# Kernel tuning notes

Measured on AMD Instinct MI355X. Metric: run time of the kernel, lower is better.

The kernel has to match this reference:

```python
import jax, jax.numpy as jnp
import numpy as np

D_MODEL = 1024
NUM_HEAD = 16
BATCH = 2
SEQ = 2048
NEG_INF = -1e9  # matches masked_fill value in the original


def setup_inputs() -> dict:
    key = jax.random.key(0)
    k1, k2, k3, k4, k5 = jax.random.split(key, 5)
    scale = 1.0 / np.sqrt(D_MODEL)
    return {
        "x": jax.random.normal(k1, (BATCH, SEQ, D_MODEL), dtype=jnp.float32),
        "q_weight": jax.random.normal(k2, (D_MODEL, D_MODEL), dtype=jnp.float32) * scale,
        "k_weight": jax.random.normal(k3, (D_MODEL, D_MODEL), dtype=jnp.float32) * scale,
        "v_weight": jax.random.normal(k4, (D_MODEL, D_MODEL), dtype=jnp.float32) * scale,
        "o_weight": jax.random.normal(k5, (D_MODEL, D_MODEL), dtype=jnp.float32) * scale,
    }


def reference(x, q_weight, k_weight, v_weight, o_weight):
    b, s, d = x.shape
    h = NUM_HEAD
    dh = d // h
    # projections: weight layout is (d_out, d_in)
    q = jnp.einsum('bsd,ed->bse', x, q_weight).reshape(b, s, h, dh).transpose(0, 2, 1, 3)
    k = jnp.einsum('bsd,ed->bse', x, k_weight).reshape(b, s, h, dh).transpose(0, 2, 1, 3)
    v = jnp.einsum('bsd,ed->bse', x, v_weight).reshape(b, s, h, dh).transpose(0, 2, 1, 3)
    scores = jnp.einsum('bhqd,bhkd->bhqk', q, k) / jnp.sqrt(jnp.asarray(dh, x.dtype))
    causal = jnp.triu(jnp.ones((s, s), dtype=bool), k=1)  # True above diagonal -> masked
    scores = jnp.where(causal, jnp.asarray(NEG_INF, x.dtype), scores)
    attn = jax.nn.softmax(scores, axis=-1)
    out = jnp.einsum('bhqk,bhkd->bhqd', attn, v)          # [b,h,s,dh]
    out = out.transpose(0, 2, 1, 3).reshape(b, s, d)       # merge heads
    return jnp.einsum('bse,de->bsd', out, o_weight)
```

## Files before the change

kernel.cpp:

```cpp
#include <hip/hip_runtime.h>

typedef short bhalf8 __attribute__((ext_vector_type(8)));
typedef short short4v __attribute__((ext_vector_type(4)));
typedef unsigned uint4v __attribute__((ext_vector_type(4)));
typedef float floatx4 __attribute__((ext_vector_type(4)));

#define D_MODEL 1024
#define SEQ     2048
#define BATCH   2
#define NHEAD   16
#define DH      64

#define GLDS(g, l) __builtin_amdgcn_global_load_lds( \
    (const __attribute__((address_space(1))) void*)(g), \
    (__attribute__((address_space(3))) void*)(l), 16, 0, 0)

static __device__ __forceinline__ short f2bf(float f) {
    unsigned u = __builtin_bit_cast(unsigned, f);
    u = (u + 0x7fffu + ((u >> 16) & 1u)) >> 16;
    return (short)u;
}
static __device__ __forceinline__ unsigned pack2(float a, float b) {
    return (unsigned)(unsigned short)f2bf(a) | ((unsigned)(unsigned short)f2bf(b) << 16);
}
static __device__ __forceinline__ unsigned cvt_pk_bf16(float lo, float hi) {
    unsigned r;
    asm("v_cvt_pk_bf16_f32 %0, %1, %2" : "=v"(r) : "v"(lo), "v"(hi));
    return r;
}

__global__ __launch_bounds__(256) void cast_all(const float* __restrict__ x,
                                                const float* __restrict__ wq,
                                                const float* __restrict__ wk,
                                                const float* __restrict__ wv,
                                                const float* __restrict__ wo,
                                                short* __restrict__ xb,
                                                short* __restrict__ wall) {
    const int bid = blockIdx.x;
    const float* s;
    short* d;
    int i;
    if (bid < 2048) {
        s = x; d = xb;
        i = (bid * 256 + threadIdx.x) * 8;
    } else {
        const int wb = bid - 2048;
        const int which = wb >> 9;
        s = (which == 0) ? wq : (which == 1) ? wk : (which == 2) ? wv : wo;
        d = wall + (size_t)which * (D_MODEL * D_MODEL);
        i = ((wb & 511) * 256 + threadIdx.x) * 8;
    }
    float4 a = *(const float4*)(s + i);
    float4 b = *(const float4*)(s + i + 4);
    uint4 u = {pack2(a.x, a.y), pack2(a.z, a.w), pack2(b.x, b.y), pack2(b.z, b.w)};
    *(uint4*)(d + i) = u;
}

#define MFMA_BF16 __builtin_amdgcn_mfma_f32_16x16x32_bf16

#define QISSUE(kt, s) do {                                                    \
    char* ab_ = pool + (s) * 16384 + (w * 32) * 64;                           \
    char* bb_ = pool + 49152 + (s) * 16384 + (w * 32) * 64;                   \
    GLDS(Ag + (size_t)(kt) * 32, ab_);                                        \
    GLDS(Ag + (size_t)(kt) * 32 + 16 * 1024, ab_ + 1024);                     \
    GLDS(Wg + (size_t)(kt) * 32, bb_);                                        \
    GLDS(Wg + (size_t)(kt) * 32 + 16 * 1024, bb_ + 1024);                     \
} while (0)

#define QCOMP(s) do {                                                         \
    const short(*As_)[32] = (const short(*)[32])(pool + (s) * 16384);         \
    const short(*Bs_)[32] = (const short(*)[32])(pool + 49152 + (s) * 16384); \
    bhalf8 af_[8], bf_[4];                                                    \
    _Pragma("unroll")                                                         \
    for (int m_ = 0; m_ < 8; ++m_)                                            \
        af_[m_] = *(const bhalf8*)&As_[wr * 128 + m_ * 16 + l16][quad * 8];   \
    _Pragma("unroll")                                                         \
    for (int n_ = 0; n_ < 4; ++n_)                                            \
        bf_[n_] = *(const bhalf8*)&Bs_[wc * 64 + n_ * 16 + l16][quad * 8];    \
    __builtin_amdgcn_s_setprio(1);                                            \
    _Pragma("unroll")                                                         \
    for (int m_ = 0; m_ < 8; ++m_)                                            \
        _Pragma("unroll")                                                     \
        for (int n_ = 0; n_ < 4; ++n_)                                        \
            acc[m_][n_] = MFMA_BF16(af_[m_], bf_[n_], acc[m_][n_], 0, 0, 0);  \
    __builtin_amdgcn_s_setprio(0);                                            \
} while (0)

__global__ __launch_bounds__(512) void gemm_qkv2(const short* __restrict__ A,
                                                 const short* __restrict__ W,
                                                 short* __restrict__ Qo,
                                                 short* __restrict__ Ko,
                                                 short* __restrict__ Vt) {
    __shared__ __align__(16) char pool[98304];
    const int t    = threadIdx.x;
    const int w    = t >> 6, lane = t & 63, quad = lane >> 4, l16 = lane & 15;
    const int wr   = w >> 2, wc = w & 3;
    const int bm   = blockIdx.x * 256;
    const int by   = (int)blockIdx.y;
    const int bn   = by * 256;

    const short* Ag = A + (size_t)(bm + w * 32 + (lane >> 2)) * 1024 + (lane & 3) * 8;
    const short* Wg = W + (size_t)(bn + w * 32 + (lane >> 2)) * 1024 + (lane & 3) * 8;

    floatx4 acc[8][4];
#pragma unroll
    for (int m = 0; m < 8; ++m)
#pragma unroll
        for (int n = 0; n < 4; ++n) {
            floatx4 z = {0.f, 0.f, 0.f, 0.f};
            acc[m][n] = z;
        }

    QISSUE(0, 0);
    QISSUE(1, 1);
    int sc_ = 0, sn_ = 2;
#pragma unroll 1
    for (int kt = 0; kt < 30; ++kt) {
        asm volatile("s_waitcnt vmcnt(4)" ::: "memory");
        __builtin_amdgcn_s_barrier();
        QISSUE(kt + 2, sn_);
        QCOMP(sc_);
        sc_ = (sc_ == 2) ? 0 : sc_ + 1;
        sn_ = (sn_ == 2) ? 0 : sn_ + 1;
    }
    asm volatile("s_waitcnt vmcnt(4)" ::: "memory");
    __builtin_amdgcn_s_barrier();
    QCOMP(sc_);
    sc_ = (sc_ == 2) ? 0 : sc_ + 1;
    asm volatile("s_waitcnt vmcnt(0)" ::: "memory");
    __builtin_amdgcn_s_barrier();
    QCOMP(sc_);

    __syncthreads();
    short (*Ct)[268] = (short(*)[268])pool;
    if (by < 8) {
        short* outp = (by < 4) ? Qo : Ko;
        const int colbase = (by < 4) ? bn : bn - 1024;
        for (int hh = 0; hh < 2; ++hh) {
            if (wr == hh) {
#pragma unroll
                for (int m = 0; m < 8; ++m)
#pragma unroll
                    for (int n = 0; n < 4; ++n)
#pragma unroll
                        for (int g = 0; g < 4; ++g)
                            Ct[m * 16 + quad * 4 + g][wc * 64 + n * 16 + l16] =
                                f2bf(acc[m][n][g]);
            }
            __syncthreads();
            {
                const int r = t >> 2, c0 = (t & 3) * 64;
#pragma unroll
                for (int p = 0; p < 8; ++p)
                    *(uint4*)(outp + (size_t)(bm + hh * 128 + r) * 1024 +
                              colbase + c0 + p * 8) =
                        *(const uint4*)&Ct[r][c0 + p * 8];
            }
            __syncthreads();
        }
    } else {
        const int nbase = bn - 2048;
        for (int hh = 0; hh < 2; ++hh) {
            if ((wc >> 1) == hh) {
#pragma unroll
                for (int m = 0; m < 8; ++m)
#pragma unroll
                    for (int n = 0; n < 4; ++n)
#pragma unroll
                        for (int g = 0; g < 4; ++g)
                            Ct[wc * 64 + n * 16 + l16 - hh * 128]
                              [wr * 128 + m * 16 + quad * 4 + g] =
                                f2bf(acc[m][n][g]);
            }
            __syncthreads();
            {
                const int r = t >> 2, c0 = (t & 3) * 64;
#pragma unroll
                for (int p = 0; p < 8; ++p)
                    *(uint4*)(Vt + (size_t)(nbase + hh * 128 + r) * 4096 +
                              bm + c0 + p * 8) =
                        *(const uint4*)&Ct[r][c0 + p * 8];
            }
            __syncthreads();
        }
    }
}

__global__ __launch_bounds__(256) void gemm_o(const short* __restrict__ A,
                                              const short* __restrict__ W,
                                              float* __restrict__ C) {
    __shared__ __align__(16) char pool[34816];
    short (*As)[64] = (short(*)[64])pool;
    short (*Bs)[64] = (short(*)[64])(pool + 16384);
    const int t    = threadIdx.x;
    const int wave = t >> 6, lane = t & 63, quad = lane >> 4, l16 = lane & 15;
    const int bm = blockIdx.x * 128, bn = blockIdx.y * 64;
    const int qm = (wave >> 1) * 64, qn = (wave & 1) * 32;

    const int lrow = lane >> 3, lcol = (lane & 7) * 8;
    const short* Ag = A + (size_t)(bm + wave * 32 + lrow) * 1024 + lcol;
    const short* Wg = W + (size_t)(bn + wave * 16 + lrow) * 1024 + lcol;
    short* Al = &As[wave * 32][0];
    short* Bl = &Bs[wave * 16][0];

    floatx4 acc[4][2];
#pragma unroll
    for (int i = 0; i < 4; ++i)
#pragma unroll
        for (int j = 0; j < 2; ++j) {
            floatx4 z = {0.f, 0.f, 0.f, 0.f};
            acc[i][j] = z;
        }

    for (int k0 = 0; k0 < 1024; k0 += 64) {
        __syncthreads();
#pragma unroll
        for (int j = 0; j < 4; ++j)
            GLDS(Ag + k0 + (size_t)j * 8 * 1024, Al + j * 8 * 64);
#pragma unroll
        for (int j = 0; j < 2; ++j)
            GLDS(Wg + k0 + (size_t)j * 8 * 1024, Bl + j * 8 * 64);
        __syncthreads();
#pragma unroll
        for (int kk = 0; kk < 64; kk += 32) {
            bhalf8 af[4], bfr[2];
#pragma unroll
            for (int im = 0; im < 4; ++im)
                af[im] = *(const bhalf8*)&As[qm + im * 16 + l16][kk + quad * 8];
#pragma unroll
            for (int jn = 0; jn < 2; ++jn)
                bfr[jn] = *(const bhalf8*)&Bs[qn + jn * 16 + l16][kk + quad * 8];
#pragma unroll
            for (int im = 0; im < 4; ++im)
#pragma unroll
                for (int jn = 0; jn < 2; ++jn)
                    acc[im][jn] = __builtin_amdgcn_mfma_f32_16x16x32_bf16(
                        af[im], bfr[jn], acc[im][jn], 0, 0, 0);
        }
    }

    __syncthreads();
    float (*Ctf)[68] = (float(*)[68])pool;
#pragma unroll
    for (int im = 0; im < 4; ++im)
#pragma unroll
        for (int jn = 0; jn < 2; ++jn)
#pragma unroll
            for (int g = 0; g < 4; ++g)
                Ctf[qm + im * 16 + quad * 4 + g][qn + jn * 16 + l16] = acc[im][jn][g];
    __syncthreads();
#pragma unroll
    for (int pass = 0; pass < 8; ++pass) {
        const int r = (t >> 4) + pass * 16;
        const int c = (t & 15) * 4;
        float4 u = *(const float4*)&Ctf[r][c];
        *(float4*)(C + (size_t)(bm + r) * 1024 + bn + c) = u;
    }
}


__global__ __launch_bounds__(512) void attn_v17(const short* __restrict__ Qo,
                                                const short* __restrict__ Ko,
                                                const short* __restrict__ Vt,
                                                short* __restrict__ Y) {
    __shared__ __align__(16) short Ks[2][64][72];
    __shared__ __align__(16) short Vs[2][64][72];

    const int t    = threadIdx.x;
    const int wave = t >> 6, lane = t & 63, quad = lane >> 4, l16 = lane & 15;
    const int bid  = (int)blockIdx.x;
    const int bh   = bid & 31;
    const int p    = (bid & 255) >> 5;
    const int qt   = (bid < 256) ? (15 - p) : p;
    const int b = bh >> 4, h = bh & 15;
    const int nc   = (qt + 1) * 2;

    const short* Qbase = Qo + (size_t)b * SEQ * 1024 + h * 64;
    const short* Kbase = Ko + (size_t)b * SEQ * 1024 + h * 64;
    const short* Vbase = Vt + (size_t)h * 64 * 4096 + (size_t)b * SEQ;

    const int sr = t >> 3;
    const int sc = (t & 7) * 8;

    const float KS = 0.125f * 1.44269504f;
    const float CB = 12.0f * 1.44269504f;

    const int qw_  = qt * 128 + wave * 16;
    const int qrow = qw_ + l16;
    const short* qr = Qbase + (size_t)qrow * 1024;
    bhalf8 qf0 = *(const bhalf8*)(qr + quad * 8);
    bhalf8 qf1 = *(const bhalf8*)(qr + 32 + quad * 8);

    float lsum = 0.f;
    floatx4 o[4];
#pragma unroll
    for (int nd = 0; nd < 4; ++nd) {
        floatx4 z = {0.f, 0.f, 0.f, 0.f};
        o[nd] = z;
    }

    uint4 kreg, vreg;
    kreg = *(const uint4*)(Kbase + (size_t)sr * 1024 + sc);
    vreg = *(const uint4*)(Vbase + (size_t)sr * 4096 + sc);
    *(uint4*)&Ks[0][sr][sc] = kreg;
    *(uint4*)&Vs[0][sr][sc] = vreg;
    if (nc > 1) {
        kreg = *(const uint4*)(Kbase + (size_t)(64 + sr) * 1024 + sc);
        vreg = *(const uint4*)(Vbase + (size_t)sr * 4096 + 64 + sc);
    }
    __syncthreads();

#pragma unroll 1
    for (int i = 0; i < nc; ++i) {
        const int buf = i & 1;
        if (i + 1 < nc) {
            *(uint4*)&Ks[buf ^ 1][sr][sc] = kreg;
            *(uint4*)&Vs[buf ^ 1][sr][sc] = vreg;
        }
        if (i + 2 < nc) {
            const int kn = (i + 2) * 64;
            kreg = *(const uint4*)(Kbase + (size_t)(kn + sr) * 1024 + sc);
            vreg = *(const uint4*)(Vbase + (size_t)sr * 4096 + kn + sc);
        }
        const int k0 = i * 64;
        if (k0 <= qw_ + 15) {
            bhalf8 kf[4][2];
#pragma unroll
            for (int jn = 0; jn < 4; ++jn) {
                kf[jn][0] = *(const bhalf8*)&Ks[buf][jn * 16 + l16][quad * 8];
                kf[jn][1] = *(const bhalf8*)&Ks[buf][jn * 16 + l16][32 + quad * 8];
            }
            floatx4 s_[4];
#pragma unroll
            for (int jn = 0; jn < 4; ++jn) {
                floatx4 z = {0.f, 0.f, 0.f, 0.f};
                z = MFMA_BF16(kf[jn][0], qf0, z, 0, 0, 0);
                z = MFMA_BF16(kf[jn][1], qf1, z, 0, 0, 0);
                s_[jn] = z;
            }
            const bool partial = (k0 + 64 > qw_);
            float e[4][4];
#pragma unroll
            for (int jn = 0; jn < 4; ++jn)
#pragma unroll
                for (int g = 0; g < 4; ++g) {
                    float v = exp2f(s_[jn][g] * KS - CB);
                    if (partial && (k0 + jn * 16 + quad * 4 + g > qrow)) v = 0.f;
                    e[jn][g] = v;
                    lsum += v;
                }
            uint4v w0 = {cvt_pk_bf16(e[0][0], e[0][1]), cvt_pk_bf16(e[0][2], e[0][3]),
                         cvt_pk_bf16(e[1][0], e[1][1]), cvt_pk_bf16(e[1][2], e[1][3])};
            uint4v w1 = {cvt_pk_bf16(e[2][0], e[2][1]), cvt_pk_bf16(e[2][2], e[2][3]),
                         cvt_pk_bf16(e[3][0], e[3][1]), cvt_pk_bf16(e[3][2], e[3][3])};
            bhalf8 af0 = __builtin_bit_cast(bhalf8, w0);
            bhalf8 af1 = __builtin_bit_cast(bhalf8, w1);
#pragma unroll
            for (int nd = 0; nd < 4; ++nd) {
                const short* vrow = &Vs[buf][nd * 16 + l16][0];
                bhalf8 vf0, vf1;
                *(short4v*)&vf0       = *(const short4v*)(vrow + quad * 4);
                *((short4v*)&vf0 + 1) = *(const short4v*)(vrow + 16 + quad * 4);
                *(short4v*)&vf1       = *(const short4v*)(vrow + 32 + quad * 4);
                *((short4v*)&vf1 + 1) = *(const short4v*)(vrow + 48 + quad * 4);
                o[nd] = MFMA_BF16(af0, vf0, o[nd], 0, 0, 0);
                o[nd] = MFMA_BF16(af1, vf1, o[nd], 0, 0, 0);
            }
        }
        __syncthreads();
    }

    lsum += __shfl_xor(lsum, 16, 64);
    lsum += __shfl_xor(lsum, 32, 64);
#pragma unroll
    for (int g = 0; g < 4; ++g) {
        const float r  = __shfl(lsum, quad * 4 + g, 64);
        const float iv = 1.0f / r;
        const int qrow_o = qw_ + quad * 4 + g;
#pragma unroll
        for (int nd = 0; nd < 4; ++nd)
            Y[(size_t)(b * SEQ + qrow_o) * 1024 + h * 64 + nd * 16 + l16] =
                f2bf(o[nd][g] * iv);
    }
}

extern "C" void kernel_launch(void* const* d_in, const int* in_sizes, int n_in,
                              void* d_out, int out_size, void* d_ws, size_t ws_size,
                              hipStream_t stream) {
    const float* x  = (const float*)d_in[0];
    const float* wq = (const float*)d_in[1];
    const float* wk = (const float*)d_in[2];
    const float* wv = (const float*)d_in[3];
    const float* wo = (const float*)d_in[4];

    short* xb   = (short*)d_ws;
    short* Qo   = xb + (size_t)4096 * 1024;
    short* Ko   = Qo + (size_t)4096 * 1024;
    short* Vt   = Ko + (size_t)4096 * 1024;
    short* wall = Vt + (size_t)1024 * 4096;
    short* wob  = wall + (size_t)3 * 1024 * 1024;

    cast_all<<<dim3(4096), 256, 0, stream>>>(x, wq, wk, wv, wo, xb, wall);
    gemm_qkv2<<<dim3(16, 12), 512, 0, stream>>>(xb, wall, Qo, Ko, Vt);
    attn_v17<<<dim3(512), 512, 0, stream>>>(Qo, Ko, Vt, xb);
    gemm_o<<<dim3(32, 16), 256, 0, stream>>>(xb, wob, (float*)d_out);
}
```

Before: 189.5 us.

## Split long causal attention tiles across two blocks and pipeline output GEMM

The attention kernel now splits the heavy query tiles (qt 8..15) into two blocks that each cover half of the key range. They exchange partial outputs and row sums through a workspace buffer, and an atomic ticket lets the second finisher merge and write the result, which balances work across 768 blocks. Separately, the output GEMM becomes a 3-stage global_load_lds pipeline with 32-wide k-steps, explicit vmcnt waits and s_setprio around the MFMAs, replacing the old load-then-compute loop. The split path adds a memset, extra global traffic for partials and a fence/atomic handshake, and it falls back to the old kernel if the workspace is too small.

```diff
diff --git a/kernel.cpp b/kernel.cpp
--- a/kernel.cpp
+++ b/kernel.cpp
@@ -186,58 +186,73 @@
     }
 }
 
-__global__ __launch_bounds__(256) void gemm_o(const short* __restrict__ A,
-                                              const short* __restrict__ W,
-                                              float* __restrict__ C) {
-    __shared__ __align__(16) char pool[34816];
-    short (*As)[64] = (short(*)[64])pool;
-    short (*Bs)[64] = (short(*)[64])(pool + 16384);
+#define OISSUE(kt, s) do {                                                    \
+    char* ab_ = pool + (s) * 12288 + w * 2048;                                \
+    char* bb_ = pool + (s) * 12288 + 8192 + w * 1024;                         \
+    GLDS(Ag + (size_t)(kt) * 32, ab_);                                        \
+    GLDS(Ag + (size_t)(kt) * 32 + 16 * 1024, ab_ + 1024);                     \
+    GLDS(Wg + (size_t)(kt) * 32, bb_);                                        \
+} while (0)
+
+#define OCOMP(s) do {                                                         \
+    const short(*As_)[32] = (const short(*)[32])(pool + (s) * 12288);         \
+    const short(*Bs_)[32] = (const short(*)[32])(pool + (s) * 12288 + 8192);  \
+    bhalf8 af_[4], bf_[2];                                                    \
+    _Pragma("unroll")                                                         \
+    for (int m_ = 0; m_ < 4; ++m_)                                            \
+        af_[m_] = *(const bhalf8*)&As_[qm + m_ * 16 + l16][quad * 8];         \
+    _Pragma("unroll")                                                         \
+    for (int n_ = 0; n_ < 2; ++n_)                                            \
+        bf_[n_] = *(const bhalf8*)&Bs_[qn + n_ * 16 + l16][quad * 8];         \
+    __builtin_amdgcn_s_setprio(1);                                            \
+    _Pragma("unroll")                                                         \
+    for (int m_ = 0; m_ < 4; ++m_)                                            \
+        _Pragma("unroll")                                                     \
+        for (int n_ = 0; n_ < 2; ++n_)                                        \
+            acc[m_][n_] = MFMA_BF16(af_[m_], bf_[n_], acc[m_][n_], 0, 0, 0);  \
+    __builtin_amdgcn_s_setprio(0);                                            \
+} while (0)
+
+__global__ __launch_bounds__(256) void gemm_o2(const short* __restrict__ A,
+                                               const short* __restrict__ W,
+                                               float* __restrict__ C) {
+    __shared__ __align__(16) char pool[36864];
     const int t    = threadIdx.x;
-    const int wave = t >> 6, lane = t & 63, quad = lane >> 4, l16 = lane & 15;
+    const int w    = t >> 6, lane = t & 63, quad = lane >> 4, l16 = lane & 15;
     const int bm = blockIdx.x * 128, bn = blockIdx.y * 64;
-    const int qm = (wave >> 1) * 64, qn = (wave & 1) * 32;
-
-    const int lrow = lane >> 3, lcol = (lane & 7) * 8;
-    const short* Ag = A + (size_t)(bm + wave * 32 + lrow) * 1024 + lcol;
-    const short* Wg = W + (size_t)(bn + wave * 16 + lrow) * 1024 + lcol;
-    short* Al = &As[wave * 32][0];
-    short* Bl = &Bs[wave * 16][0];
+    const int qm = (w >> 1) * 64, qn = (w & 1) * 32;
+
+    const short* Ag = A + (size_t)(bm + w * 32 + (lane >> 2)) * 1024 + (lane & 3) * 8;
+    const short* Wg = W + (size_t)(bn + w * 16 + (lane >> 2)) * 1024 + (lane & 3) * 8;
 
     floatx4 acc[4][2];
 #pragma unroll
-    for (int i = 0; i < 4; ++i)
-#pragma unroll
-        for (int j = 0; j < 2; ++j) {
+    for (int m = 0; m < 4; ++m)
+#pragma unroll
+        for (int n = 0; n < 2; ++n) {
             floatx4 z = {0.f, 0.f, 0.f, 0.f};
-            acc[i][j] = z;
+            acc[m][n] = z;
         }
 
-    for (int k0 = 0; k0 < 1024; k0 += 64) {
-        __syncthreads();
-#pragma unroll
-        for (int j = 0; j < 4; ++j)
-            GLDS(Ag + k0 + (size_t)j * 8 * 1024, Al + j * 8 * 64);
-#pragma unroll
-        for (int j = 0; j < 2; ++j)
-            GLDS(Wg + k0 + (size_t)j * 8 * 1024, Bl + j * 8 * 64);
-        __syncthreads();
-#pragma unroll
-        for (int kk = 0; kk < 64; kk += 32) {
-            bhalf8 af[4], bfr[2];
-#pragma unroll
-            for (int im = 0; im < 4; ++im)
-                af[im] = *(const bhalf8*)&As[qm + im * 16 + l16][kk + quad * 8];
-#pragma unroll
-            for (int jn = 0; jn < 2; ++jn)
-                bfr[jn] = *(const bhalf8*)&Bs[qn + jn * 16 + l16][kk + quad * 8];
-#pragma unroll
-            for (int im = 0; im < 4; ++im)
-#pragma unroll
-                for (int jn = 0; jn < 2; ++jn)
-                    acc[im][jn] = __builtin_amdgcn_mfma_f32_16x16x32_bf16(
-                        af[im], bfr[jn], acc[im][jn], 0, 0, 0);
-        }
-    }
+    OISSUE(0, 0);
+    OISSUE(1, 1);
+    int sc_ = 0, sn_ = 2;
+#pragma unroll 1
+    for (int kt = 0; kt < 30; ++kt) {
+        asm volatile("s_waitcnt vmcnt(3)" ::: "memory");
+        __builtin_amdgcn_s_barrier();
+        OISSUE(kt + 2, sn_);
+        OCOMP(sc_);
+        sc_ = (sc_ == 2) ? 0 : sc_ + 1;
+        sn_ = (sn_ == 2) ? 0 : sn_ + 1;
+    }
+    asm volatile("s_waitcnt vmcnt(3)" ::: "memory");
+    __builtin_amdgcn_s_barrier();
+    OCOMP(sc_);
+    sc_ = (sc_ == 2) ? 0 : sc_ + 1;
+    asm volatile("s_waitcnt vmcnt(0)" ::: "memory");
+    __builtin_amdgcn_s_barrier();
+    OCOMP(sc_);
 
     __syncthreads();
     float (*Ctf)[68] = (float(*)[68])pool;
@@ -258,14 +273,175 @@
     }
 }
 
-
-__global__ __launch_bounds__(512) void attn_v17(const short* __restrict__ Qo,
+#define ATTN_BODY(KERN_NC, KERN_KBASE)                                        \
+    uint4 kreg, vreg;                                                         \
+    kreg = *(const uint4*)(Kbase + (size_t)((KERN_KBASE) + sr) * 1024 + sc);  \
+    vreg = *(const uint4*)(Vbase + (size_t)sr * 4096 + (KERN_KBASE) + sc);    \
+    *(uint4*)&Ks[0][sr][sc] = kreg;                                           \
+    *(uint4*)&Vs[0][sr][sc] = vreg;                                           \
+    if ((KERN_NC) > 1) {                                                      \
+        kreg = *(const uint4*)(Kbase + (size_t)((KERN_KBASE) + 64 + sr) * 1024 + sc); \
+        vreg = *(const uint4*)(Vbase + (size_t)sr * 4096 + (KERN_KBASE) + 64 + sc);   \
+    }                                                                         \
+    __syncthreads();                                                          \
+    _Pragma("unroll 1")                                                       \
+    for (int i = 0; i < (KERN_NC); ++i) {                                     \
+        const int buf = i & 1;                                                \
+        if (i + 1 < (KERN_NC)) {                                              \
+            *(uint4*)&Ks[buf ^ 1][sr][sc] = kreg;                             \
+            *(uint4*)&Vs[buf ^ 1][sr][sc] = vreg;                             \
+        }                                                                     \
+        if (i + 2 < (KERN_NC)) {                                              \
+            const int kn = (KERN_KBASE) + (i + 2) * 64;                       \
+            kreg = *(const uint4*)(Kbase + (size_t)(kn + sr) * 1024 + sc);    \
+            vreg = *(const uint4*)(Vbase + (size_t)sr * 4096 + kn + sc);      \
+        }                                                                     \
+        const int k0 = (KERN_KBASE) + i * 64;                                 \
+        if (k0 <= qw_ + 15) {                                                 \
+            bhalf8 kf[4][2];                                                  \
+            _Pragma("unroll")                                                 \
+            for (int jn = 0; jn < 4; ++jn) {                                  \
+                kf[jn][0] = *(const bhalf8*)&Ks[buf][jn * 16 + l16][quad * 8];\
+                kf[jn][1] = *(const bhalf8*)&Ks[buf][jn * 16 + l16][32 + quad * 8]; \
+            }                                                                 \
+            floatx4 s_[4];                                                    \
+            _Pragma("unroll")                                                 \
+            for (int jn = 0; jn < 4; ++jn) {                                  \
+                floatx4 z = {0.f, 0.f, 0.f, 0.f};                             \
+                z = MFMA_BF16(kf[jn][0], qf0, z, 0, 0, 0);                    \
+                z = MFMA_BF16(kf[jn][1], qf1, z, 0, 0, 0);                    \
+                s_[jn] = z;                                                   \
+            }                                                                 \
+            const bool partial = (k0 + 64 > qw_);                             \
+            float e[4][4];                                                    \
+            _Pragma("unroll")                                                 \
+            for (int jn = 0; jn < 4; ++jn)                                    \
+                _Pragma("unroll")                                             \
+                for (int g = 0; g < 4; ++g) {                                 \
+                    float v = exp2f(s_[jn][g] * KS - CB);                     \
+                    if (partial && (k0 + jn * 16 + quad * 4 + g > qrow)) v = 0.f; \
+                    e[jn][g] = v;                                             \
+                    lsum += v;                                                \
+                }                                                             \
+            uint4v w0 = {cvt_pk_bf16(e[0][0], e[0][1]), cvt_pk_bf16(e[0][2], e[0][3]), \
+                         cvt_pk_bf16(e[1][0], e[1][1]), cvt_pk_bf16(e[1][2], e[1][3])}; \
+            uint4v w1 = {cvt_pk_bf16(e[2][0], e[2][1]), cvt_pk_bf16(e[2][2], e[2][3]), \
+                         cvt_pk_bf16(e[3][0], e[3][1]), cvt_pk_bf16(e[3][2], e[3][3])}; \
+            bhalf8 af0 = __builtin_bit_cast(bhalf8, w0);                      \
+            bhalf8 af1 = __builtin_bit_cast(bhalf8, w1);                      \
+            _Pragma("unroll")                                                 \
+            for (int nd = 0; nd < 4; ++nd) {                                  \
+                const short* vrow = &Vs[buf][nd * 16 + l16][0];               \
+                bhalf8 vf0, vf1;                                              \
+                *(short4v*)&vf0       = *(const short4v*)(vrow + quad * 4);   \
+                *((short4v*)&vf0 + 1) = *(const short4v*)(vrow + 16 + quad * 4); \
+                *(short4v*)&vf1       = *(const short4v*)(vrow + 32 + quad * 4); \
+                *((short4v*)&vf1 + 1) = *(const short4v*)(vrow + 48 + quad * 4); \
+                o[nd] = MFMA_BF16(af0, vf0, o[nd], 0, 0, 0);                  \
+                o[nd] = MFMA_BF16(af1, vf1, o[nd], 0, 0, 0);                  \
+            }                                                                 \
+        }                                                                     \
+        __syncthreads();                                                      \
+    }                                                                         \
+    lsum += __shfl_xor(lsum, 16, 64);                                         \
+    lsum += __shfl_xor(lsum, 32, 64);
+
+#define ATTN_STORE_Y()                                                        \
+    _Pragma("unroll")                                                         \
+    for (int g = 0; g < 4; ++g) {                                             \
+        const float r  = __shfl(lsum, quad * 4 + g, 64);                      \
+        const float iv = 1.0f / r;                                            \
+        const int qrow_o = qw_ + quad * 4 + g;                                \
+        _Pragma("unroll")                                                     \
+        for (int nd = 0; nd < 4; ++nd)                                        \
+            Y[(size_t)(b * SEQ + qrow_o) * 1024 + h * 64 + nd * 16 + l16] =   \
+                f2bf(o[nd][g] * iv);                                          \
+    }
+
+__global__ __launch_bounds__(512) void attn_v18(const short* __restrict__ Qo,
                                                 const short* __restrict__ Ko,
                                                 const short* __restrict__ Vt,
-                                                short* __restrict__ Y) {
+                                                short* __restrict__ Y,
+                                                float* __restrict__ Pw,
+                                                int* __restrict__ flags) {
     __shared__ __align__(16) short Ks[2][64][72];
     __shared__ __align__(16) short Vs[2][64][72];
 
+    const int t    = threadIdx.x;
+    const int wave = t >> 6, lane = t & 63, quad = lane >> 4, l16 = lane & 15;
+    const int bid  = (int)blockIdx.x;
+    const int bh   = bid & 31;
+    const int g8   = (bid & 255) >> 5;
+    const int grp  = bid >> 8;
+    int qt, nc, kbase, half;
+    if (grp == 0)      { qt = 15 - g8; nc = 16 - g8; kbase = 0;               half = 0; }
+    else if (grp == 1) { qt = 15 - g8; nc = 16 - g8; kbase = (16 - g8) * 64;  half = 1; }
+    else               { qt = g8;      nc = 2 * (g8 + 1); kbase = 0;          half = -1; }
+    const int b = bh >> 4, h = bh & 15;
+
+    const short* Qbase = Qo + (size_t)b * SEQ * 1024 + h * 64;
+    const short* Kbase = Ko + (size_t)b * SEQ * 1024 + h * 64;
+    const short* Vbase = Vt + (size_t)h * 64 * 4096 + (size_t)b * SEQ;
+
+    const int sr = t >> 3;
+    const int sc = (t & 7) * 8;
+
+    const float KS = 0.125f * 1.44269504f;
+    const float CB = 12.0f * 1.44269504f;
+
+    const int qw_  = qt * 128 + wave * 16;
+    const int qrow = qw_ + l16;
+    const short* qr = Qbase + (size_t)qrow * 1024;
+    bhalf8 qf0 = *(const bhalf8*)(qr + quad * 8);
+    bhalf8 qf1 = *(const bhalf8*)(qr + 32 + quad * 8);
+
+    float lsum = 0.f;
+    floatx4 o[4];
+#pragma unroll
+    for (int nd = 0; nd < 4; ++nd) {
+        floatx4 z = {0.f, 0.f, 0.f, 0.f};
+        o[nd] = z;
+    }
+
+    ATTN_BODY(nc, kbase);
+
+    if (half < 0) {
+        ATTN_STORE_Y();
+        return;
+    }
+
+    const int tidx = bh * 8 + (qt - 8);
+    float* pb = Pw + (size_t)(tidx * 2 + half) * 8320;
+#pragma unroll
+    for (int g = 0; g < 4; ++g)
+#pragma unroll
+        for (int nd = 0; nd < 4; ++nd)
+            pb[(wave * 16 + quad * 4 + g) * 64 + nd * 16 + l16] = o[nd][g];
+    if (quad == 0) pb[8192 + wave * 16 + l16] = lsum;
+    __threadfence();
+    __syncthreads();
+    int* tick = (int*)&Ks[0][0][0];
+    if (t == 0) *tick = atomicAdd(&flags[tidx], 1);
+    __syncthreads();
+    if (*tick == 1) {
+        __threadfence();
+        const float* qb = Pw + (size_t)(tidx * 2 + (1 - half)) * 8320;
+#pragma unroll
+        for (int g = 0; g < 4; ++g)
+#pragma unroll
+            for (int nd = 0; nd < 4; ++nd)
+                o[nd][g] += qb[(wave * 16 + quad * 4 + g) * 64 + nd * 16 + l16];
+        lsum += qb[8192 + wave * 16 + l16];
+        ATTN_STORE_Y();
+    }
+}
+
+__global__ __launch_bounds__(512) void attn_v17f(const short* __restrict__ Qo,
+                                                 const short* __restrict__ Ko,
+                                                 const short* __restrict__ Vt,
+                                                 short* __restrict__ Y) {
+    __shared__ __align__(16) short Ks[2][64][72];
+    __shared__ __align__(16) short Vs[2][64][72];
     const int t    = threadIdx.x;
     const int wave = t >> 6, lane = t & 63, quad = lane >> 4, l16 = lane & 15;
     const int bid  = (int)blockIdx.x;
@@ -274,23 +450,17 @@
     const int qt   = (bid < 256) ? (15 - p) : p;
     const int b = bh >> 4, h = bh & 15;
     const int nc   = (qt + 1) * 2;
-
     const short* Qbase = Qo + (size_t)b * SEQ * 1024 + h * 64;
     const short* Kbase = Ko + (size_t)b * SEQ * 1024 + h * 64;
     const short* Vbase = Vt + (size_t)h * 64 * 4096 + (size_t)b * SEQ;
-
-    const int sr = t >> 3;
-    const int sc = (t & 7) * 8;
-
+    const int sr = t >> 3, sc = (t & 7) * 8;
     const float KS = 0.125f * 1.44269504f;
     const float CB = 12.0f * 1.44269504f;
-
     const int qw_  = qt * 128 + wave * 16;
     const int qrow = qw_ + l16;
     const short* qr = Qbase + (size_t)qrow * 1024;
     bhalf8 qf0 = *(const bhalf8*)(qr + quad * 8);
     bhalf8 qf1 = *(const bhalf8*)(qr + 32 + quad * 8);
-
     float lsum = 0.f;
     floatx4 o[4];
 #pragma unroll
@@ -298,90 +468,8 @@
         floatx4 z = {0.f, 0.f, 0.f, 0.f};
         o[nd] = z;
     }
-
-    uint4 kreg, vreg;
-    kreg = *(const uint4*)(Kbase + (size_t)sr * 1024 + sc);
-    vreg = *(const uint4*)(Vbase + (size_t)sr * 4096 + sc);
-    *(uint4*)&Ks[0][sr][sc] = kreg;
-    *(uint4*)&Vs[0][sr][sc] = vreg;
-    if (nc > 1) {
-        kreg = *(const uint4*)(Kbase + (size_t)(64 + sr) * 1024 + sc);
-        vreg = *(const uint4*)(Vbase + (size_t)sr * 4096 + 64 + sc);
-    }
-    __syncthreads();
-
-#pragma unroll 1
-    for (int i = 0; i < nc; ++i) {
-        const int buf = i & 1;
-        if (i + 1 < nc) {
-            *(uint4*)&Ks[buf ^ 1][sr][sc] = kreg;
-            *(uint4*)&Vs[buf ^ 1][sr][sc] = vreg;
-        }
-        if (i + 2 < nc) {
-            const int kn = (i + 2) * 64;
-            kreg = *(const uint4*)(Kbase + (size_t)(kn + sr) * 1024 + sc);
-            vreg = *(const uint4*)(Vbase + (size_t)sr * 4096 + kn + sc);
-        }
-        const int k0 = i * 64;
-        if (k0 <= qw_ + 15) {
-            bhalf8 kf[4][2];
-#pragma unroll
-            for (int jn = 0; jn < 4; ++jn) {
-                kf[jn][0] = *(const bhalf8*)&Ks[buf][jn * 16 + l16][quad * 8];
-                kf[jn][1] = *(const bhalf8*)&Ks[buf][jn * 16 + l16][32 + quad * 8];
-            }
-            floatx4 s_[4];
-#pragma unroll
-            for (int jn = 0; jn < 4; ++jn) {
-                floatx4 z = {0.f, 0.f, 0.f, 0.f};
-                z = MFMA_BF16(kf[jn][0], qf0, z, 0, 0, 0);
-                z = MFMA_BF16(kf[jn][1], qf1, z, 0, 0, 0);
-                s_[jn] = z;
-            }
-            const bool partial = (k0 + 64 > qw_);
-            float e[4][4];
-#pragma unroll
-            for (int jn = 0; jn < 4; ++jn)
-#pragma unroll
-                for (int g = 0; g < 4; ++g) {
-                    float v = exp2f(s_[jn][g] * KS - CB);
-                    if (partial && (k0 + jn * 16 + quad * 4 + g > qrow)) v = 0.f;
-                    e[jn][g] = v;
-                    lsum += v;
-                }
-            uint4v w0 = {cvt_pk_bf16(e[0][0], e[0][1]), cvt_pk_bf16(e[0][2], e[0][3]),
-                         cvt_pk_bf16(e[1][0], e[1][1]), cvt_pk_bf16(e[1][2], e[1][3])};
-            uint4v w1 = {cvt_pk_bf16(e[2][0], e[2][1]), cvt_pk_bf16(e[2][2], e[2][3]),
-                         cvt_pk_bf16(e[3][0], e[3][1]), cvt_pk_bf16(e[3][2], e[3][3])};
-            bhalf8 af0 = __builtin_bit_cast(bhalf8, w0);
-            bhalf8 af1 = __builtin_bit_cast(bhalf8, w1);
-#pragma unroll
-            for (int nd = 0; nd < 4; ++nd) {
-                const short* vrow = &Vs[buf][nd * 16 + l16][0];
-                bhalf8 vf0, vf1;
-                *(short4v*)&vf0       = *(const short4v*)(vrow + quad * 4);
-                *((short4v*)&vf0 + 1) = *(const short4v*)(vrow + 16 + quad * 4);
-                *(short4v*)&vf1       = *(const short4v*)(vrow + 32 + quad * 4);
-                *((short4v*)&vf1 + 1) = *(const short4v*)(vrow + 48 + quad * 4);
-                o[nd] = MFMA_BF16(af0, vf0, o[nd], 0, 0, 0);
-                o[nd] = MFMA_BF16(af1, vf1, o[nd], 0, 0, 0);
-            }
-        }
-        __syncthreads();
-    }
-
-    lsum += __shfl_xor(lsum, 16, 64);
-    lsum += __shfl_xor(lsum, 32, 64);
-#pragma unroll
-    for (int g = 0; g < 4; ++g) {
-        const float r  = __shfl(lsum, quad * 4 + g, 64);
-        const float iv = 1.0f / r;
-        const int qrow_o = qw_ + quad * 4 + g;
-#pragma unroll
-        for (int nd = 0; nd < 4; ++nd)
-            Y[(size_t)(b * SEQ + qrow_o) * 1024 + h * 64 + nd * 16 + l16] =
-                f2bf(o[nd][g] * iv);
-    }
+    ATTN_BODY(nc, 0);
+    ATTN_STORE_Y();
 }
 
 extern "C" void kernel_launch(void* const* d_in, const int* in_sizes, int n_in,
@@ -399,9 +487,17 @@
     short* Vt   = Ko + (size_t)4096 * 1024;
     short* wall = Vt + (size_t)1024 * 4096;
     short* wob  = wall + (size_t)3 * 1024 * 1024;
+    float* Pw   = (float*)(wob + (size_t)1024 * 1024);
+    int*   flags = (int*)((char*)Pw + (size_t)512 * 8320 * 4);
+    const size_t needed = (size_t)(41943040) + (size_t)512 * 8320 * 4 + 1024;
 
     cast_all<<<dim3(4096), 256, 0, stream>>>(x, wq, wk, wv, wo, xb, wall);
     gemm_qkv2<<<dim3(16, 12), 512, 0, stream>>>(xb, wall, Qo, Ko, Vt);
-    attn_v17<<<dim3(512), 512, 0, stream>>>(Qo, Ko, Vt, xb);
-    gemm_o<<<dim3(32, 16), 256, 0, stream>>>(xb, wob, (float*)d_out);
-}
+    if (ws_size >= needed) {
+        hipMemsetAsync(flags, 0, 256 * sizeof(int), stream);
+        attn_v18<<<dim3(768), 512, 0, stream>>>(Qo, Ko, Vt, xb, Pw, flags);
+    } else {
+        attn_v17f<<<dim3(512), 512, 0, stream>>>(Qo, Ko, Vt, xb);
+    }
+    gemm_o2<<<dim3(32, 16), 256, 0, stream>>>(xb, wob, (float*)d_out);
+}
```

After: 369.0 us. +94.7%, slower.
